# Kernel optimization log

Hardware: AMD Instinct MI355X
Metric: run time of the kernel (lower is better)

The kernel has to match this reference:

```python
import jax, jax.numpy as jnp
import numpy as np

D_MODEL = 1024
N_Q = 16
N_KV = 4
HEAD = 64
T = 4096
B = 1


def setup_inputs() -> dict:
    key = jax.random.key(0)
    ks = jax.random.split(key, 5)
    q_dim = N_Q * HEAD
    kv_dim = N_KV * HEAD
    s = 0.02
    return {
        "x": jax.random.normal(ks[0], (B, T, D_MODEL), dtype=jnp.float32),
        "W_q": jax.random.normal(ks[1], (D_MODEL, q_dim), dtype=jnp.float32) * s,
        "W_k": jax.random.normal(ks[2], (D_MODEL, kv_dim), dtype=jnp.float32) * s,
        "W_v": jax.random.normal(ks[3], (D_MODEL, kv_dim), dtype=jnp.float32) * s,
        "W_o": jax.random.normal(ks[4], (q_dim, D_MODEL), dtype=jnp.float32) * s,
    }


def reference(x, W_q, W_k, W_v, W_o):
    Bsz, Tlen, _ = x.shape
    n_q_per_kv = N_Q // N_KV
    scale = jnp.asarray(np.sqrt(HEAD), x.dtype)
    # projections, split heads: (B, T, H*D) -> (B, H, T, D)
    q = (x @ W_q).reshape(Bsz, Tlen, N_Q, HEAD).transpose(0, 2, 1, 3)
    k = (x @ W_k).reshape(Bsz, Tlen, N_KV, HEAD).transpose(0, 2, 1, 3)
    v = (x @ W_v).reshape(Bsz, Tlen, N_KV, HEAD).transpose(0, 2, 1, 3)
    # GQA: duplicate KV heads to match query heads (repeat_interleave on head dim)
    k = jnp.repeat(k, n_q_per_kv, axis=1)
    v = jnp.repeat(v, n_q_per_kv, axis=1)
    attn = jnp.einsum("bhqd,bhkd->bhqk", q, k) / scale  # (B, H, T, T)
    causal = jnp.tril(jnp.ones((Tlen, Tlen), dtype=bool))
    attn = jnp.where(causal[None, None], attn, -jnp.inf)
    attn = jax.nn.softmax(attn, axis=-1)
    out = jnp.einsum("bhqk,bhkd->bhqd", attn, v)  # (B, H, T, D)
    out = out.transpose(0, 2, 1, 3).reshape(Bsz, Tlen, N_Q * HEAD)
    return out @ W_o
```

## Files before the change

kernel.cpp:

```cpp
#include <hip/hip_runtime.h>

typedef __bf16 bf16;
typedef __bf16 bf16x4 __attribute__((ext_vector_type(4)));
typedef __bf16 bf16x8 __attribute__((ext_vector_type(8)));
typedef float  f32x4  __attribute__((ext_vector_type(4)));

#define DEV __device__ __forceinline__

#if __has_builtin(__builtin_amdgcn_exp2f)
#define EXP2(x) __builtin_amdgcn_exp2f(x)
#else
#define EXP2(x) exp2f(x)
#endif

DEV void gload16(const void* g, void* l) {
  __builtin_amdgcn_global_load_lds((const __attribute__((address_space(1))) void*)g,
                                   (__attribute__((address_space(3))) void*)l, 16, 0, 0);
}

DEV f32x4 mfma16(bf16x8 a, bf16x8 b, f32x4 c) {
  return __builtin_amdgcn_mfma_f32_16x16x32_bf16(a, b, c, 0, 0, 0);
}

#define QSCALE 0.18033688011112042f

__global__ __launch_bounds__(256) void cast_x_kernel(const float* __restrict__ x,
                                                     bf16* __restrict__ xb) {
  int i = blockIdx.x * 256 + threadIdx.x;
  f32x4 v = ((const f32x4*)x)[i];
  bf16x4 o = {(bf16)v.x, (bf16)v.y, (bf16)v.z, (bf16)v.w};
  ((bf16x4*)xb)[i] = o;
}

__global__ __launch_bounds__(256) void wtrans_kernel(const float* __restrict__ sQ,
                                                     const float* __restrict__ sK,
                                                     const float* __restrict__ sV,
                                                     bf16* __restrict__ dst) {
  __shared__ float tile[32][33];
  int k0 = blockIdx.x * 32, n0 = blockIdx.y * 32;
  int tx = threadIdx.x & 31, ty = threadIdx.x >> 5;
  const float* src; int ld, nb;
  if (n0 < 1024)      { src = sQ; ld = 1024; nb = 0; }
  else if (n0 < 1280) { src = sK; ld = 256;  nb = 1024; }
  else                { src = sV; ld = 256;  nb = 1280; }
#pragma unroll
  for (int i = 0; i < 4; i++) {
    int r = ty + 8 * i;
    tile[r][tx] = src[(size_t)(k0 + r) * ld + (n0 - nb + tx)];
  }
  __syncthreads();
#pragma unroll
  for (int i = 0; i < 4; i++) {
    int r = ty + 8 * i;
    dst[(size_t)(n0 + r) * 1024 + k0 + tx] = (bf16)tile[tx][r];
  }
}

template <int MODE>
__global__ __launch_bounds__(256) void gemm_kernel(const bf16* __restrict__ A,
                                                   const bf16* __restrict__ B,
                                                   float* __restrict__ Cf,
                                                   bf16* __restrict__ qkbuf,
                                                   bf16* __restrict__ vtbuf, int N) {
  constexpr int K = 1024;
  __shared__ bf16 Al[2][64 * 32];
  __shared__ bf16 Bl[2][128 * 32];
  int tid = threadIdx.x;
  int w = tid >> 6, lane = tid & 63;
  int g = lane >> 4, r15 = lane & 15;
  int wr = w >> 1, wc = w & 1;
  int m0 = blockIdx.y * 64, n0 = blockIdx.x * 128;

  int sra = 16 * w + (lane >> 2);
  int srb = 32 * w + (lane >> 2);
  int ss = lane & 3;
  const bf16* a0 = A + (size_t)(m0 + sra) * K + 8 * (ss ^ ((sra >> 1) & 3));
  const bf16* b0 = B + (size_t)(n0 + srb) * K + 8 * (ss ^ ((srb >> 1) & 3));
  const bf16* b1 = B + (size_t)(n0 + srb + 16) * K + 8 * (ss ^ (((srb + 16) >> 1) & 3));

#define GSTAGE(kk_, b_) do { \
    char* ad = (char*)Al[b_] + w * 1024; \
    char* bd = (char*)Bl[b_] + w * 2048; \
    gload16(a0 + (kk_), ad); \
    gload16(b0 + (kk_), bd); \
    gload16(b1 + (kk_), bd + 1024); \
  } while (0)

  GSTAGE(0, 0);
  __syncthreads();

  f32x4 acc[2][4] = {};
  for (int kk = 0; kk < K; kk += 32) {
    int cur = (kk >> 5) & 1;
    if (kk + 32 < K) GSTAGE(kk + 32, cur ^ 1);
    bf16x8 af[2], bb[4];
#pragma unroll
    for (int i = 0; i < 2; i++) {
      int m = 32 * wr + 16 * i + r15;
      af[i] = *(const bf16x8*)((const char*)Al[cur] + m * 64 + 16 * (g ^ ((m >> 1) & 3)));
    }
#pragma unroll
    for (int i = 0; i < 4; i++) {
      int n = 64 * wc + 16 * i + r15;
      bb[i] = *(const bf16x8*)((const char*)Bl[cur] + n * 64 + 16 * (g ^ ((n >> 1) & 3)));
    }
    __builtin_amdgcn_s_setprio(1);
#pragma unroll
    for (int mi = 0; mi < 2; mi++)
#pragma unroll
      for (int ni = 0; ni < 4; ni++)
        acc[mi][ni] = mfma16(af[mi], bb[ni], acc[mi][ni]);
    __builtin_amdgcn_s_setprio(0);
    __syncthreads();
  }

  if (MODE == 0) {
#pragma unroll
    for (int mi = 0; mi < 2; mi++) {
      int mg = m0 + 32 * wr + 16 * mi + 4 * g;
#pragma unroll
      for (int ni = 0; ni < 4; ni++) {
        int ng = n0 + 64 * wc + 16 * ni + r15;
#pragma unroll
        for (int r = 0; r < 4; r++)
          Cf[(size_t)(mg + r) * N + ng] = acc[mi][ni][r];
      }
    }
  } else {
    if (n0 < 1280) {
      float qs = (n0 < 1024) ? QSCALE : 1.0f;
#pragma unroll
      for (int mi = 0; mi < 2; mi++) {
        int tg = m0 + 32 * wr + 16 * mi + 4 * g;
#pragma unroll
        for (int ni = 0; ni < 4; ni++) {
          int ng = n0 + 64 * wc + 16 * ni + r15;
#pragma unroll
          for (int r = 0; r < 4; r++)
            qkbuf[(size_t)(tg + r) * 1280 + ng] = (bf16)(acc[mi][ni][r] * qs);
        }
      }
    } else {
#pragma unroll
      for (int mi = 0; mi < 2; mi++) {
        int tg = m0 + 32 * wr + 16 * mi + 4 * g;
#pragma unroll
        for (int ni = 0; ni < 4; ni++) {
          int vcol = n0 + 64 * wc + 16 * ni + r15 - 1280;
          bf16x4 pk = {(bf16)acc[mi][ni][0], (bf16)acc[mi][ni][1],
                       (bf16)acc[mi][ni][2], (bf16)acc[mi][ni][3]};
          *(bf16x4*)(vtbuf + (size_t)vcol * 4096 + tg) = pk;
        }
      }
    }
  }
#undef GSTAGE
}

__global__ __launch_bounds__(256) void attn_kernel(const bf16* __restrict__ qk,
                                                   const bf16* __restrict__ vt,
                                                   bf16* __restrict__ out) {
  __shared__ bf16 Kt[2][64 * 64];
  __shared__ bf16 Vt[2][64 * 64];
  __shared__ bf16 Pl[4][16][72];
  int tid = threadIdx.x, w = tid >> 6, lane = tid & 63;
  int g = lane >> 4, r15 = lane & 15;
  int p = blockIdx.x;
  int h = blockIdx.y, kh = h >> 2;
  int na = p + 1, tot = 65;
  int qw = 64 * p + 16 * w;

  bf16x8 bq[2];
#pragma unroll
  for (int ks = 0; ks < 2; ks++)
    bq[ks] = *(const bf16x8*)(qk + (size_t)(qw + r15) * 1280 + h * 64 + 32 * ks + 8 * g);

  float l_run = 0.f;
  f32x4 oacc[4] = {};

  int sw8 = 8 * ((lane & 7) ^ (lane >> 3));
  const bf16* kbase = qk + 1024 + (size_t)kh * 64 + (size_t)(16 * w + (lane >> 3)) * 1280 + sw8;
  const bf16* vbase = vt + ((size_t)(kh * 64 + 16 * w + (lane >> 3))) * 4096 + sw8;

#define STAGE(t0_, b_) do { \
    char* kd = (char*)Kt[b_] + w * 2048; \
    char* vd = (char*)Vt[b_] + w * 2048; \
    gload16(kbase + (size_t)(t0_) * 1280, kd); \
    gload16(kbase + (size_t)(t0_) * 1280 + (size_t)8 * 1280, kd + 1024); \
    gload16(vbase + (t0_), vd); \
    gload16(vbase + (t0_) + 8 * 4096, vd + 1024); \
  } while (0)

  STAGE(0, 0);
  __syncthreads();

  for (int it = 0; it < tot; ++it) {
    int cur = it & 1;
    int t0 = (it < na) ? 64 * it : 64 * (it - na);
    if (it + 1 < tot) {
      int tn = (it + 1 < na) ? 64 * (it + 1) : 64 * (it + 1 - na);
      STAGE(tn, cur ^ 1);
    }
    if (it == na) {
      float lsum = l_run;
      lsum += __shfl_xor(lsum, 16);
      lsum += __shfl_xor(lsum, 32);
      float linv = 1.0f / lsum;
      float li[4];
#pragma unroll
      for (int r = 0; r < 4; r++) li[r] = __shfl(linv, 4 * g + r);
#pragma unroll
      for (int ni = 0; ni < 4; ni++)
#pragma unroll
        for (int r = 0; r < 4; r++)
          out[(size_t)(qw + 4 * g + r) * 1024 + h * 64 + 16 * ni + r15] =
              (bf16)(oacc[ni][r] * li[r]);
      l_run = 0.f;
#pragma unroll
      for (int ni = 0; ni < 4; ni++) oacc[ni] = (f32x4){0.f, 0.f, 0.f, 0.f};
      qw = 64 * (63 - p) + 16 * w;
#pragma unroll
      for (int ks = 0; ks < 2; ks++)
        bq[ks] = *(const bf16x8*)(qk + (size_t)(qw + r15) * 1280 + h * 64 + 32 * ks + 8 * g);
    }
    bool need_mask = (it == na - 1) || (it == tot - 1);
    const char* Kc = (const char*)Kt[cur];
    const char* Vc = (const char*)Vt[cur];

    f32x4 s[4];
    __builtin_amdgcn_s_setprio(1);
#pragma unroll
    for (int mi = 0; mi < 4; mi++) {
      int kv = 16 * mi + r15;
      bf16x8 k0f = *(const bf16x8*)(Kc + kv * 128 + 16 * (g ^ (kv & 7)));
      bf16x8 k1f = *(const bf16x8*)(Kc + kv * 128 + 16 * ((4 + g) ^ (kv & 7)));
      f32x4 z = {};
      z = mfma16(k0f, bq[0], z);
      z = mfma16(k1f, bq[1], z);
      s[mi] = z;
    }
    __builtin_amdgcn_s_setprio(0);

    int qg = qw + r15;
    float psum = 0.f;
    bf16 pb[16];
#pragma unroll
    for (int mi = 0; mi < 4; mi++)
#pragma unroll
      for (int r = 0; r < 4; r++) {
        float v = s[mi][r];
        if (need_mask) {
          int kvg = t0 + 16 * mi + 4 * g + r;
          v = (kvg > qg) ? -1e30f : v;
        }
        float pp = EXP2(v);
        psum += pp;
        pb[4 * mi + r] = (bf16)pp;
      }
    l_run += psum;

#pragma unroll
    for (int mi = 0; mi < 4; mi++) {
      bf16x4 pk = {pb[4 * mi], pb[4 * mi + 1], pb[4 * mi + 2], pb[4 * mi + 3]};
      *(bf16x4*)((char*)&Pl[w][r15][0] + mi * 32 + g * 8) = pk;
    }
    bf16x8 ap0 = *(const bf16x8*)((const char*)&Pl[w][r15][0] + 16 * g);
    bf16x8 ap1 = *(const bf16x8*)((const char*)&Pl[w][r15][0] + 64 + 16 * g);
    __builtin_amdgcn_s_setprio(1);
#pragma unroll
    for (int ni = 0; ni < 4; ni++) {
      int d = 16 * ni + r15;
      bf16x8 bv0 = *(const bf16x8*)(Vc + d * 128 + 16 * (g ^ (d & 7)));
      bf16x8 bv1 = *(const bf16x8*)(Vc + d * 128 + 16 * ((4 + g) ^ (d & 7)));
      oacc[ni] = mfma16(ap0, bv0, oacc[ni]);
      oacc[ni] = mfma16(ap1, bv1, oacc[ni]);
    }
    __builtin_amdgcn_s_setprio(0);
    __syncthreads();
  }
#undef STAGE

  float lsum = l_run;
  lsum += __shfl_xor(lsum, 16);
  lsum += __shfl_xor(lsum, 32);
  float linv = 1.0f / lsum;
  float li[4];
#pragma unroll
  for (int r = 0; r < 4; r++) li[r] = __shfl(linv, 4 * g + r);
#pragma unroll
  for (int ni = 0; ni < 4; ni++)
#pragma unroll
    for (int r = 0; r < 4; r++)
      out[(size_t)(qw + 4 * g + r) * 1024 + h * 64 + 16 * ni + r15] =
          (bf16)(oacc[ni][r] * li[r]);
}

extern "C" void kernel_launch(void* const* d_in, const int* in_sizes, int n_in,
                              void* d_out, int out_size, void* d_ws, size_t ws_size,
                              hipStream_t stream) {
  const float* x  = (const float*)d_in[0];
  const float* Wq = (const float*)d_in[1];
  const float* Wk = (const float*)d_in[2];
  const float* Wv = (const float*)d_in[3];
  const float* Wo = (const float*)d_in[4];
  float* out = (float*)d_out;
  char* ws = (char*)d_ws;
  bf16* xb    = (bf16*)(ws);
  bf16* wqkvt = (bf16*)(ws + 8388608);
  bf16* wot   = (bf16*)(ws + 11534336);
  bf16* qkbuf = (bf16*)(ws + 13631488);
  bf16* vtb   = (bf16*)(ws + 24117248);

  cast_x_kernel<<<4096, 256, 0, stream>>>(x, xb);
  wtrans_kernel<<<dim3(32, 48), 256, 0, stream>>>(Wq, Wk, Wv, wqkvt);
  wtrans_kernel<<<dim3(32, 32), 256, 0, stream>>>(Wo, Wo, Wo, wot);
  gemm_kernel<1><<<dim3(12, 64), 256, 0, stream>>>(xb, wqkvt, nullptr, qkbuf, vtb, 1536);
  attn_kernel<<<dim3(32, 16), 256, 0, stream>>>(qkbuf, vtb, xb);
  gemm_kernel<0><<<dim3(8, 64), 256, 0, stream>>>(xb, wot, out, nullptr, nullptr, 1024);
}
```

Baseline: 207.8 us.

## Replace paired causal tiles with one-tile-per-block, longest-first scheduling

The attention kernel used to pair query tile p with tile 63-p inside one block so every block did 65 KV iterations. Now each block handles a single 64-row query tile and the grid is ordered with the longest tiles (largest tI) dispatched first. This doubles the block count to 1024 and removes the mid-loop finalize/reload branch, relying on the hardware scheduler to balance the uneven causal work. The cost is more block launches, repeated Q loads and prologue overhead, and a tail of short blocks.

```diff
diff --git a/kernel.cpp b/kernel.cpp
--- a/kernel.cpp
+++ b/kernel.cpp
@@ -165,10 +165,11 @@
   __shared__ bf16 Pl[4][16][72];
   int tid = threadIdx.x, w = tid >> 6, lane = tid & 63;
   int g = lane >> 4, r15 = lane & 15;
-  int p = blockIdx.x;
-  int h = blockIdx.y, kh = h >> 2;
-  int na = p + 1, tot = 65;
-  int qw = 64 * p + 16 * w;
+  int j = blockIdx.x;
+  int h = j & 15, tI = 63 - (j >> 4);
+  int kh = h >> 2;
+  int na = tI + 1;
+  int qw = 64 * tI + 16 * w;
 
   bf16x8 bq[2];
 #pragma unroll
@@ -194,36 +195,11 @@
   STAGE(0, 0);
   __syncthreads();
 
-  for (int it = 0; it < tot; ++it) {
+  for (int it = 0; it < na; ++it) {
     int cur = it & 1;
-    int t0 = (it < na) ? 64 * it : 64 * (it - na);
-    if (it + 1 < tot) {
-      int tn = (it + 1 < na) ? 64 * (it + 1) : 64 * (it + 1 - na);
-      STAGE(tn, cur ^ 1);
-    }
-    if (it == na) {
-      float lsum = l_run;
-      lsum += __shfl_xor(lsum, 16);
-      lsum += __shfl_xor(lsum, 32);
-      float linv = 1.0f / lsum;
-      float li[4];
-#pragma unroll
-      for (int r = 0; r < 4; r++) li[r] = __shfl(linv, 4 * g + r);
-#pragma unroll
-      for (int ni = 0; ni < 4; ni++)
-#pragma unroll
-        for (int r = 0; r < 4; r++)
-          out[(size_t)(qw + 4 * g + r) * 1024 + h * 64 + 16 * ni + r15] =
-              (bf16)(oacc[ni][r] * li[r]);
-      l_run = 0.f;
-#pragma unroll
-      for (int ni = 0; ni < 4; ni++) oacc[ni] = (f32x4){0.f, 0.f, 0.f, 0.f};
-      qw = 64 * (63 - p) + 16 * w;
-#pragma unroll
-      for (int ks = 0; ks < 2; ks++)
-        bq[ks] = *(const bf16x8*)(qk + (size_t)(qw + r15) * 1280 + h * 64 + 32 * ks + 8 * g);
-    }
-    bool need_mask = (it == na - 1) || (it == tot - 1);
+    int t0 = 64 * it;
+    if (it + 1 < na) STAGE(64 * (it + 1), cur ^ 1);
+    bool need_mask = (it == na - 1);
     const char* Kc = (const char*)Kt[cur];
     const char* Vc = (const char*)Vt[cur];
 
@@ -315,6 +291,6 @@
   wtrans_kernel<<<dim3(32, 48), 256, 0, stream>>>(Wq, Wk, Wv, wqkvt);
   wtrans_kernel<<<dim3(32, 32), 256, 0, stream>>>(Wo, Wo, Wo, wot);
   gemm_kernel<1><<<dim3(12, 64), 256, 0, stream>>>(xb, wqkvt, nullptr, qkbuf, vtb, 1536);
-  attn_kernel<<<dim3(32, 16), 256, 0, stream>>>(qkbuf, vtb, xb);
+  attn_kernel<<<dim3(1024), 256, 0, stream>>>(qkbuf, vtb, xb);
   gemm_kernel<0><<<dim3(8, 64), 256, 0, stream>>>(xb, wot, out, nullptr, nullptr, 1024);
 }
```

Measured after the change: 184.5 us. -11.2%, faster.
